# Kernel tuning notes

Hardware: AMD Instinct MI355X
Metric: run time of the kernel (lower is better)

## Reference

```python
import jax, jax.numpy as jnp
import numpy as np

EPS = 1e-5
NUM_HEADS = 4
HEAD_DIM = 64
NUM_STEPS = 3


def layernorm(x, g, b):
    mu = jnp.mean(x, axis=-1, keepdims=True)
    var = jnp.mean((x - mu) ** 2, axis=-1, keepdims=True)
    return (x - mu) / jnp.sqrt(var + EPS) * g + b


def entmax15(x):
    # exact alpha=1.5 entmax along last axis (Peters et al. 2019)
    n = x.shape[-1]
    x = x - jnp.max(x, axis=-1, keepdims=True)
    x = x / 2.0
    srt = -jnp.sort(-x, axis=-1)                      # descending
    rho = jnp.arange(1, n + 1, dtype=x.dtype)
    cs = jnp.cumsum(srt, axis=-1)
    cs2 = jnp.cumsum(srt * srt, axis=-1)
    mean = cs / rho
    ss = cs2 - mean * cs                              # k * (mean_sq - mean^2)
    delta = (1.0 - ss) / rho
    d = jnp.clip(delta, 0.0)
    safe = jnp.where(d > 0, d, 1.0)
    tau = mean - jnp.where(d > 0, jnp.sqrt(safe), 0.0)
    support = (tau <= srt).astype(jnp.int32)
    k_star = jnp.sum(support, axis=-1, keepdims=True) - 1
    tau_star = jnp.take_along_axis(tau, k_star, axis=-1)
    p = jnp.clip(x - tau_star, 0.0)
    return p * p


def setup_inputs() -> dict:
    key = jax.random.key(0)
    ks = jax.random.split(key, 8)
    B, S, Dh = 2, 512, 2048
    N, Dm = 8192, 1024
    T = NUM_HEADS * HEAD_DIM  # 256
    hidden = jax.random.normal(ks[0], (B, S, Dh), dtype=jnp.float32)
    memory = jax.random.normal(ks[1], (N, Dm), dtype=jnp.float32)
    Wq = jax.random.normal(ks[2], (Dh, T), dtype=jnp.float32) * 0.02
    Wk = jax.random.normal(ks[3], (Dm, T), dtype=jnp.float32) * 0.02
    Wv = jax.random.normal(ks[4], (Dm, T), dtype=jnp.float32) * 0.02
    Wo = jax.random.normal(ks[5], (T, Dh), dtype=jnp.float32) * 0.02
    log_beta = jnp.full((NUM_HEADS,), float(np.log(1.0 / np.sqrt(HEAD_DIM))), dtype=jnp.float32)
    g_s = jnp.ones((Dh,), jnp.float32)
    b_s = jnp.zeros((Dh,), jnp.float32)
    g_m = jnp.ones((Dm,), jnp.float32)
    b_m = jnp.zeros((Dm,), jnp.float32)
    return {"hidden": hidden, "memory": memory, "Wq": Wq, "Wk": Wk, "Wv": Wv,
            "Wo": Wo, "log_beta": log_beta, "g_s": g_s, "b_s": b_s,
            "g_m": g_m, "b_m": b_m}


def reference(hidden, memory, Wq, Wk, Wv, Wo, log_beta, g_s, b_s, g_m, b_m):
    B, S, _ = hidden.shape
    N = memory.shape[0]
    H, D = NUM_HEADS, HEAD_DIM
    Q = layernorm(hidden, g_s, b_s) @ Wq                         # [B,S,H*D]
    mem_n = layernorm(memory, g_m, b_m)
    K = (mem_n @ Wk).reshape(N, H, D).transpose(1, 0, 2)         # [H,N,D]
    V = (mem_n @ Wv).reshape(N, H, D).transpose(1, 0, 2)         # [H,N,D]
    xi = Q.reshape(B, S, H, D).transpose(0, 2, 1, 3)             # [B,H,S,D]
    beta = jnp.exp(log_beta)[None, :, None, None]                # [1,H,1,1]
    for _ in range(NUM_STEPS):
        scores = jnp.einsum('bhsd,hnd->bhsn', xi, K) * beta      # [B,H,S,N]
        w = entmax15(scores)
        xi = jnp.einsum('bhsn,hnd->bhsd', w, V)
    converged = xi.transpose(0, 2, 1, 3).reshape(B, S, H * D)
    output = converged @ Wo                                      # [B,S,hidden_dim]
    return output, converged
```

## Files before the change

kernel.cpp:

```cpp
#include <hip/hip_runtime.h>
#include <math.h>

typedef _Float16 f16;
typedef f16 f16x8 __attribute__((ext_vector_type(8)));
typedef float f32x4 __attribute__((ext_vector_type(4)));

#define QSCALE 16384.0f
#define QINV 6.103515625e-5f
#define QOFF 2.5f

__device__ __forceinline__ float wred_add(float v) {
#pragma unroll
  for (int off = 32; off >= 1; off >>= 1) v += __shfl_xor(v, off, 64);
  return v;
}
__device__ __forceinline__ float wred_max(float v) {
#pragma unroll
  for (int off = 32; off >= 1; off >>= 1) v = fmaxf(v, __shfl_xor(v, off, 64));
  return v;
}

__global__ __launch_bounds__(256) void ln_stats_kernel(
    const float* __restrict__ X, int cols, float* __restrict__ mu,
    float* __restrict__ rs) {
  int row = blockIdx.x, tid = threadIdx.x;
  const float4* xr = (const float4*)(X + (size_t)row * cols);
  int nv = cols >> 10;
  float s = 0.f, s2 = 0.f;
  for (int v = 0; v < nv; ++v) {
    float4 x4 = xr[tid + (v << 8)];
    s += x4.x + x4.y + x4.z + x4.w;
    s2 += x4.x * x4.x + x4.y * x4.y + x4.z * x4.z + x4.w * x4.w;
  }
  s = wred_add(s);
  s2 = wred_add(s2);
  __shared__ float rb[8];
  int wid = tid >> 6, lane = tid & 63;
  if (lane == 0) { rb[wid] = s; rb[4 + wid] = s2; }
  __syncthreads();
  if (tid == 0) {
    float S = rb[0] + rb[1] + rb[2] + rb[3];
    float S2 = rb[4] + rb[5] + rb[6] + rb[7];
    float m = S / (float)cols;
    float var = S2 / (float)cols - m * m;
    mu[row] = m;
    rs[row] = 1.f / sqrtf(var + 1e-5f);
  }
}

__global__ __launch_bounds__(256) void split_a_kernel(
    const float* __restrict__ X, const float* __restrict__ mu,
    const float* __restrict__ rs, f16x8* __restrict__ Ah,
    f16x8* __restrict__ Al, int M, int Kd, int lay) {
  int blk = blockIdx.x * 4 + (threadIdx.x >> 6);
  int l = threadIdx.x & 63;
  int nmt = M >> 4;
  int kc = blk / nmt, mt = blk - kc * nmt;
  int m = mt * 16 + (l & 15);
  int k = kc * 32 + ((l >> 4) << 3);
  const float* src;
  if (lay == 0) {
    src = X + (size_t)m * Kd + k;
  } else {
    int b = m >> 9, s = m & 511, hh = k >> 6, d = k & 63;
    src = X + ((((size_t)b * 4 + hh) * 512 + s) << 6) + d;
  }
  float mm = mu ? mu[m] : 0.f;
  float rr = rs ? rs[m] : 1.f;
  f16x8 hi, lo;
#pragma unroll
  for (int j = 0; j < 8; ++j) {
    float v = (src[j] - mm) * rr;
    f16 hv = (f16)v;
    hi[j] = hv;
    lo[j] = (f16)((v - (float)hv) * 512.f);
  }
  size_t o = ((size_t)blk << 6) + l;
  Ah[o] = hi;
  Al[o] = lo;
}

__global__ __launch_bounds__(256) void split_w_kernel(
    const float* __restrict__ W, const float* __restrict__ g,
    f16x8* __restrict__ Bh, f16x8* __restrict__ Bl, int Kd, int N) {
  int blk = blockIdx.x * 4 + (threadIdx.x >> 6);
  int l = threadIdx.x & 63;
  int nnt = N >> 4;
  int kc = blk / nnt, nt = blk - kc * nnt;
  int n = nt * 16 + (l & 15);
  int k0 = kc * 32 + ((l >> 4) << 3);
  f16x8 hi, lo;
#pragma unroll
  for (int j = 0; j < 8; ++j) {
    float v = W[(size_t)(k0 + j) * N + n];
    if (g) v *= g[k0 + j];
    f16 hv = (f16)v;
    hi[j] = hv;
    lo[j] = (f16)((v - (float)hv) * 512.f);
  }
  size_t o = ((size_t)blk << 6) + l;
  Bh[o] = hi;
  Bl[o] = lo;
}

__global__ __launch_bounds__(256) void wcol3_kernel(
    const float* __restrict__ Wq, const float* __restrict__ bq,
    const float* __restrict__ Wk, const float* __restrict__ bk,
    const float* __restrict__ Wv, const float* __restrict__ bv,
    float* __restrict__ vbq, float* __restrict__ vbk,
    float* __restrict__ vbv) {
  int which = blockIdx.z;
  const float* W = which == 0 ? Wq : (which == 1 ? Wk : Wv);
  const float* b = which == 0 ? bq : (which == 1 ? bk : bv);
  float* vb = which == 0 ? vbq : (which == 1 ? vbk : vbv);
  int Kd = which == 0 ? 2048 : 1024;
  int t = threadIdx.x;
  int kpb = Kd >> 4;
  int k0 = blockIdx.y * kpb;
  float s = 0.f;
  for (int k = k0; k < k0 + kpb; ++k) s = fmaf(b[k], W[(size_t)k * 256 + t], s);
  atomicAdd(&vb[t], s);
}

__global__ __launch_bounds__(256) void gemm_mfma_kernel(
    const f16x8* __restrict__ Ah, const f16x8* __restrict__ Al,
    const f16x8* __restrict__ Bh, const f16x8* __restrict__ Bl,
    const float* __restrict__ vb, float* __restrict__ outf,
    f16x8* __restrict__ o16a, f16x8* __restrict__ o16b, int M, int N, int nk,
    int out_mode) {
  __shared__ __align__(16) float Ts[64][68];
  const int tid = threadIdx.x;
  const int w = tid >> 6, l = tid & 63;
  const int ql = l & 15, g = l >> 4;
  const int bn = blockIdx.x, bm = blockIdx.y;
  const size_t astr = ((size_t)(M >> 4)) << 6;
  const size_t bstr = ((size_t)(N >> 4)) << 6;
  const f16x8* aph = Ah + (((size_t)(bm * 4 + w)) << 6) + l;
  const f16x8* apl = Al + (((size_t)(bm * 4 + w)) << 6) + l;
  const f16x8* bph = Bh + (((size_t)(bn * 4)) << 6) + l;
  const f16x8* bpl = Bl + (((size_t)(bn * 4)) << 6) + l;

  f32x4 cm[4], cx[4];
#pragma unroll
  for (int nf = 0; nf < 4; ++nf) {
    cm[nf] = (f32x4){0.f, 0.f, 0.f, 0.f};
    cx[nf] = (f32x4){0.f, 0.f, 0.f, 0.f};
  }

  f16x8 a0h = aph[0], a0l = apl[0];
  f16x8 b0h[4], b0l[4];
#pragma unroll
  for (int nf = 0; nf < 4; ++nf) {
    b0h[nf] = bph[nf << 6];
    b0l[nf] = bpl[nf << 6];
  }

  for (int kc = 0; kc < nk - 1; ++kc) {
    const size_t ao = (size_t)(kc + 1) * astr;
    const size_t bo = (size_t)(kc + 1) * bstr;
    f16x8 a1h = aph[ao], a1l = apl[ao];
    f16x8 b1h[4], b1l[4];
#pragma unroll
    for (int nf = 0; nf < 4; ++nf) {
      b1h[nf] = bph[bo + (nf << 6)];
      b1l[nf] = bpl[bo + (nf << 6)];
    }
#pragma unroll
    for (int nf = 0; nf < 4; ++nf) {
      cm[nf] = __builtin_amdgcn_mfma_f32_16x16x32_f16(a0h, b0h[nf], cm[nf], 0, 0, 0);
      cx[nf] = __builtin_amdgcn_mfma_f32_16x16x32_f16(a0h, b0l[nf], cx[nf], 0, 0, 0);
      cx[nf] = __builtin_amdgcn_mfma_f32_16x16x32_f16(a0l, b0h[nf], cx[nf], 0, 0, 0);
    }
    a0h = a1h;
    a0l = a1l;
#pragma unroll
    for (int nf = 0; nf < 4; ++nf) {
      b0h[nf] = b1h[nf];
      b0l[nf] = b1l[nf];
    }
  }
#pragma unroll
  for (int nf = 0; nf < 4; ++nf) {
    cm[nf] = __builtin_amdgcn_mfma_f32_16x16x32_f16(a0h, b0h[nf], cm[nf], 0, 0, 0);
    cx[nf] = __builtin_amdgcn_mfma_f32_16x16x32_f16(a0h, b0l[nf], cx[nf], 0, 0, 0);
    cx[nf] = __builtin_amdgcn_mfma_f32_16x16x32_f16(a0l, b0h[nf], cx[nf], 0, 0, 0);
  }

  float vbc[4] = {0.f, 0.f, 0.f, 0.f};
  if (vb) {
#pragma unroll
    for (int nf = 0; nf < 4; ++nf) vbc[nf] = vb[bn * 64 + nf * 16 + ql];
  }

  if (out_mode == 0) {
#pragma unroll
    for (int nf = 0; nf < 4; ++nf)
#pragma unroll
      for (int r = 0; r < 4; ++r) {
        float val = fmaf(cx[nf][r], 0.001953125f, cm[nf][r]) + vbc[nf];
        int m = bm * 64 + w * 16 + (g << 2) + r;
        int n = bn * 64 + nf * 16 + ql;
        int b = m >> 9, s = m & 511, hh = n >> 6, d = n & 63;
        outf[((((size_t)b * 4 + hh) * 512 + s) << 6) + d] = val;
      }
  } else if (out_mode == 3) {
#pragma unroll
    for (int nf = 0; nf < 4; ++nf)
#pragma unroll
      for (int r = 0; r < 4; ++r) {
        float val = fmaf(cx[nf][r], 0.001953125f, cm[nf][r]) + vbc[nf];
        int m = bm * 64 + w * 16 + (g << 2) + r;
        int n = bn * 64 + nf * 16 + ql;
        outf[(size_t)m * N + n] = val;
      }
  } else {
#pragma unroll
    for (int nf = 0; nf < 4; ++nf)
#pragma unroll
      for (int r = 0; r < 4; ++r)
        Ts[w * 16 + (g << 2) + r][nf * 16 + ql] =
            fmaf(cx[nf][r], 0.001953125f, cm[nf][r]) + vbc[nf];
    __syncthreads();
    if (out_mode == 4) {
#pragma unroll
      for (int i = 0; i < 2; ++i) {
        int slot = tid + (i << 8);
        int blk = slot >> 6, l2 = slot & 63;
        int ktl = blk >> 1, dc = blk & 1;
        int key = (ktl << 4) + (l2 & 15);
        int db = (dc << 5) + ((l2 >> 4) << 3);
        f16x8 hi, lo;
#pragma unroll
        for (int j = 0; j < 8; ++j) {
          float v = Ts[key][db + j];
          f16 hv = (f16)v;
          hi[j] = hv;
          lo[j] = (f16)((v - (float)hv) * 512.f);
        }
        size_t o = (((size_t)(bn * 512 + bm * 4 + ktl) * 2 + dc) << 6) + l2;
        o16a[o] = hi;
        o16b[o] = lo;
      }
    } else {
#pragma unroll
      for (int i = 0; i < 2; ++i) {
        int slot = tid + (i << 8);
        int blk = slot >> 6, l2 = slot & 63;
        int dt = blk >> 1, kcl = blk & 1;
        int keyb = (kcl << 5) + ((l2 >> 4) << 3);
        int d = (dt << 4) + (l2 & 15);
        f16x8 v8;
#pragma unroll
        for (int j = 0; j < 8; ++j) v8[j] = (f16)Ts[keyb + j][d];
        size_t o = (((size_t)(bn * 4 + dt) * 256 + bm * 2 + kcl) << 6) + l2;
        o16a[o] = v8;
      }
    }
  }
}

__global__ __launch_bounds__(512) void hop_score_kernel(
    const float* __restrict__ xi_in, const f16x8* __restrict__ Khi,
    const f16x8* __restrict__ Klo, const float* __restrict__ log_beta,
    unsigned short* __restrict__ Y) {
  __shared__ float xiq[16][64];
  __shared__ float mxb[8][16];
  __shared__ float mxs[16];
  const int tid = threadIdx.x;
  const int w = tid >> 6, l = tid & 63;
  const int ql = l & 15, g = l >> 4;
  const int bh = blockIdx.x & 7, qtile = blockIdx.x >> 3;
  const int h = bh & 3;
  const size_t base_io = ((size_t)bh * 512 + qtile * 16) * 64;

  float beta = expf(log_beta[h]);
  for (int i = tid; i < 1024; i += 512)
    xiq[i >> 6][i & 63] = xi_in[base_io + i] * beta;
  __syncthreads();

  f16x8 xh0, xh1, xl0, xl1;
#pragma unroll
  for (int j = 0; j < 8; ++j) {
    float x0 = xiq[ql][(g << 3) + j];
    float x1 = xiq[ql][32 + (g << 3) + j];
    f16 h0 = (f16)x0, h1 = (f16)x1;
    xh0[j] = h0; xl0[j] = (f16)((x0 - (float)h0) * 512.f);
    xh1[j] = h1; xl1[j] = (f16)((x1 - (float)h1) * 512.f);
  }

  const f16x8* kb = Khi + (size_t)h * 65536 + l;
  const f16x8* kl = Klo + (size_t)h * 65536 + l;
  const int kt0 = w * 64;

  float mymax = -3.4e38f;
  for (int kt = kt0; kt < kt0 + 2; ++kt) {
    f32x4 c = {0.f, 0.f, 0.f, 0.f};
    c = __builtin_amdgcn_mfma_f32_16x16x32_f16(kb[(size_t)kt * 128], xh0, c, 0, 0, 0);
    c = __builtin_amdgcn_mfma_f32_16x16x32_f16(kb[(size_t)kt * 128 + 64], xh1, c, 0, 0, 0);
    mymax = fmaxf(fmaxf(fmaxf(c[0], c[1]), fmaxf(c[2], c[3])), mymax);
  }
  mymax = fmaxf(mymax, __shfl_xor(mymax, 16, 64));
  mymax = fmaxf(mymax, __shfl_xor(mymax, 32, 64));
  if (l < 16) mxb[w][ql] = mymax;
  __syncthreads();
  if (tid < 16) {
    float m = mxb[0][tid];
#pragma unroll
    for (int ww = 1; ww < 8; ++ww) m = fmaxf(m, mxb[ww][tid]);
    mxs[tid] = m;
  }
  __syncthreads();
  const float mh = mxs[ql] * 0.5f;
  const float qc = QOFF * QSCALE + 0.5f - mh * QSCALE;

  const size_t Ybase = (size_t)(bh * 32 + qtile) * 131072;
  for (int kt = kt0; kt < kt0 + 64; ++kt) {
    f16x8 a0 = kb[(size_t)kt * 128], a1 = kb[(size_t)kt * 128 + 64];
    f16x8 b0 = kl[(size_t)kt * 128], b1 = kl[(size_t)kt * 128 + 64];
    f32x4 cm = {0.f, 0.f, 0.f, 0.f}, cx = {0.f, 0.f, 0.f, 0.f};
    cm = __builtin_amdgcn_mfma_f32_16x16x32_f16(a0, xh0, cm, 0, 0, 0);
    cm = __builtin_amdgcn_mfma_f32_16x16x32_f16(a1, xh1, cm, 0, 0, 0);
    cx = __builtin_amdgcn_mfma_f32_16x16x32_f16(b0, xh0, cx, 0, 0, 0);
    cx = __builtin_amdgcn_mfma_f32_16x16x32_f16(a0, xl0, cx, 0, 0, 0);
    cx = __builtin_amdgcn_mfma_f32_16x16x32_f16(b1, xh1, cx, 0, 0, 0);
    cx = __builtin_amdgcn_mfma_f32_16x16x32_f16(a1, xl1, cx, 0, 0, 0);
    ushort4 uv;
    unsigned short* up = (unsigned short*)&uv;
#pragma unroll
    for (int r = 0; r < 4; ++r) {
      float s = fmaf(cx[r], 0.001953125f, cm[r]);
      float uq = fmaf(s, 8192.0f, qc);
      uq = fminf(fmaxf(uq, 0.f), 65535.f);
      up[r] = (unsigned short)(int)uq;
    }
    *(ushort4*)&Y[Ybase + (size_t)(kt >> 1) * 512 + ql * 32 + (kt & 1) * 16 +
                  (g << 2)] = uv;
  }
}

__global__ __launch_bounds__(256) void hop_tau_kernel(
    const unsigned short* __restrict__ Y, float* __restrict__ tau) {
  const int row = blockIdx.x;
  const int bh = row >> 9, qi = row & 511;
  const int qtile = qi >> 4, ql = qi & 15;
  const size_t yb = (size_t)(bh * 32 + qtile) * 131072 + ql * 32;
  const int t = threadIdx.x;
  const uint4* p = (const uint4*)(Y + yb + (size_t)t * 512);
  float y[32];
#pragma unroll
  for (int v = 0; v < 4; ++v) {
    uint4 u = p[v];
    unsigned a[4] = {u.x, u.y, u.z, u.w};
#pragma unroll
    for (int e = 0; e < 4; ++e) {
      y[v * 8 + e * 2] = fmaf((float)(a[e] & 0xffffu), QINV, -QOFF);
      y[v * 8 + e * 2 + 1] = fmaf((float)(a[e] >> 16), QINV, -QOFF);
    }
  }
  __shared__ float redm[4];
  __shared__ float rb[5][4];
  __shared__ float rb3[3][4][3];
  const int wi = t >> 6, lane = t & 63;

  {
    float m = y[0];
#pragma unroll
    for (int i = 1; i < 32; ++i) m = fmaxf(m, y[i]);
    m = wred_max(m);
    if (lane == 0) redm[wi] = m;
  }
  __syncthreads();
  const float ymax =
      fmaxf(fmaxf(redm[0], redm[1]), fmaxf(redm[2], redm[3]));

  float lo = ymax - 1.001f, hi = ymax;
#pragma unroll 1
  for (int it = 0; it < 5; ++it) {
    float tv = 0.5f * (lo + hi);
    float f = 0.f;
#pragma unroll
    for (int i = 0; i < 32; ++i) {
      float d = fmaxf(y[i] - tv, 0.f);
      f = fmaf(d, d, f);
    }
    f = wred_add(f);
    if (lane == 0) rb[it][wi] = f;
    __syncthreads();
    float tot = rb[it][0] + rb[it][1] + rb[it][2] + rb[it][3];
    if (tot >= 1.f) lo = tv; else hi = tv;
  }

  float tc = lo;
#pragma unroll 1
  for (int it = 0; it < 3; ++it) {
    float kk = 0.f, s1 = 0.f, s2 = 0.f;
#pragma unroll
    for (int i = 0; i < 32; ++i) {
      if (y[i] > tc) { kk += 1.f; s1 += y[i]; s2 = fmaf(y[i], y[i], s2); }
    }
    kk = wred_add(kk);
    s1 = wred_add(s1);
    s2 = wred_add(s2);
    if (lane == 0) { rb3[it][wi][0] = kk; rb3[it][wi][1] = s1; rb3[it][wi][2] = s2; }
    __syncthreads();
    float K = rb3[it][0][0] + rb3[it][1][0] + rb3[it][2][0] + rb3[it][3][0];
    float S1 = rb3[it][0][1] + rb3[it][1][1] + rb3[it][2][1] + rb3[it][3][1];
    float S2 = rb3[it][0][2] + rb3[it][1][2] + rb3[it][2][2] + rb3[it][3][2];
    if (K >= 0.5f) {
      float mean = S1 / K;
      float ss = fmaf(-mean, S1, S2);
      float delta = (1.f - ss) / K;
      tc = delta > 0.f ? mean - sqrtf(delta) : mean;
    }
  }
  if (t == 0) tau[row] = tc;
}

__global__ __launch_bounds__(512) void hop_pv_kernel(
    const unsigned short* __restrict__ Y, const f16x8* __restrict__ Vp,
    const float* __restrict__ tau, float* __restrict__ xi_out) {
  __shared__ float outp[8][16][64];
  __shared__ float taus[16];
  const int tid = threadIdx.x;
  const int w = tid >> 6, l = tid & 63;
  const int ql = l & 15, g = l >> 4;
  const int bh = blockIdx.x & 7, qtile = blockIdx.x >> 3;
  const int h = bh & 3;
  const size_t base_io = ((size_t)bh * 512 + qtile * 16) * 64;

  if (tid < 16) taus[tid] = tau[bh * 512 + qtile * 16 + tid];
  __syncthreads();
  const float t1 = taus[ql];
  const size_t Ybase = (size_t)(bh * 32 + qtile) * 131072;
  const f16x8* vb = Vp + (size_t)h * 65536 + l;

  f32x4 m2[4];
#pragma unroll
  for (int dt = 0; dt < 4; ++dt) m2[dt] = (f32x4){0.f, 0.f, 0.f, 0.f};

  for (int kc = 0; kc < 32; ++kc) {
    const int chunk = w * 32 + kc;
    uint4 uv = *(const uint4*)(Y + Ybase + (size_t)chunk * 512 + ql * 32 +
                               (g << 3));
    unsigned a[4] = {uv.x, uv.y, uv.z, uv.w};
    f16x8 a2;
#pragma unroll
    for (int e = 0; e < 4; ++e) {
      float y0 = fmaf((float)(a[e] & 0xffffu), QINV, -QOFF);
      float y1 = fmaf((float)(a[e] >> 16), QINV, -QOFF);
      float p0 = fmaxf(y0 - t1, 0.f);
      float p1 = fmaxf(y1 - t1, 0.f);
      a2[e * 2] = (f16)(p0 * p0);
      a2[e * 2 + 1] = (f16)(p1 * p1);
    }
#pragma unroll
    for (int dt = 0; dt < 4; ++dt) {
      f16x8 vf = vb[(((size_t)dt * 256 + chunk) << 6)];
      m2[dt] = __builtin_amdgcn_mfma_f32_16x16x32_f16(a2, vf, m2[dt], 0, 0, 0);
    }
  }
#pragma unroll
  for (int dt = 0; dt < 4; ++dt)
#pragma unroll
    for (int r = 0; r < 4; ++r)
      outp[w][(g << 2) + r][dt * 16 + ql] = m2[dt][r];
  __syncthreads();
  for (int i = tid; i < 1024; i += 512) {
    float s = 0.f;
#pragma unroll
    for (int ww = 0; ww < 8; ++ww) s += outp[ww][i >> 6][i & 63];
    xi_out[base_io + i] = s;
  }
}

__global__ __launch_bounds__(256) void conv_copy_kernel(
    const float* __restrict__ xi, float* __restrict__ out) {
  int o4 = blockIdx.x * 256 + threadIdx.x;
  int o = o4 << 2;
  int dd = o & 63, hq = (o >> 6) & 3, sq = (o >> 8) & 511, bq = o >> 17;
  float4 v =
      *(const float4*)&xi[((((size_t)bq << 2) + hq) * 512 + sq) * 64 + dd];
  *(float4*)&out[o] = v;
}

extern "C" void kernel_launch(void* const* d_in, const int* in_sizes, int n_in,
                              void* d_out, int out_size, void* d_ws,
                              size_t ws_size, hipStream_t stream) {
  (void)in_sizes; (void)n_in; (void)out_size; (void)ws_size;
  const float* hidden = (const float*)d_in[0];
  const float* memory = (const float*)d_in[1];
  const float* Wq = (const float*)d_in[2];
  const float* Wk = (const float*)d_in[3];
  const float* Wv = (const float*)d_in[4];
  const float* Wo = (const float*)d_in[5];
  const float* log_beta = (const float*)d_in[6];
  const float* g_s = (const float*)d_in[7];
  const float* b_s = (const float*)d_in[8];
  const float* g_m = (const float*)d_in[9];
  const float* b_m = (const float*)d_in[10];
  float* out = (float*)d_out;

  float* ws = (float*)d_ws;
  float* mu_h = ws;
  float* rs_h = ws + 1024;
  float* mu_m = ws + 2048;
  float* rs_m = ws + 10240;
  float* xiA = ws + 18432;
  float* xiB = ws + 280576;
  float* vb_q = ws + 542720;
  float* vb_k = ws + 542976;
  float* vb_v = ws + 543232;
  float* tau = ws + 543488;
  f16x8* Khi = (f16x8*)(ws + 548864);
  f16x8* Klo = Khi + 262144;
  f16x8* Vp = Klo + 262144;
  f16x8* Bqh = Vp + 262144;
  f16x8* Bql = Bqh + 65536;
  f16x8* Bkh = Bql + 65536;
  f16x8* Bkl = Bkh + 32768;
  f16x8* Bvh = Bkl + 32768;
  f16x8* Bvl = Bvh + 32768;
  f16x8* Boh = Bvl + 32768;
  f16x8* Bol = Boh + 65536;
  unsigned short* Y = (unsigned short*)(Bol + 65536);
  f16x8* Amh = (f16x8*)Y;
  f16x8* Aml = Amh + 1048576;
  f16x8* Ahh = Aml + 1048576;
  f16x8* Ahl = Ahh + 262144;
  f16x8* Axh = Ahl + 262144;
  f16x8* Axl = Axh + 32768;

  ln_stats_kernel<<<1024, 256, 0, stream>>>(hidden, 2048, mu_h, rs_h);
  ln_stats_kernel<<<8192, 256, 0, stream>>>(memory, 1024, mu_m, rs_m);
  hipMemsetAsync(vb_q, 0, 3 * 256 * sizeof(float), stream);

  split_a_kernel<<<1024, 256, 0, stream>>>(hidden, mu_h, rs_h, Ahh, Ahl, 1024,
                                           2048, 0);
  split_a_kernel<<<4096, 256, 0, stream>>>(memory, mu_m, rs_m, Amh, Aml, 8192,
                                           1024, 0);
  split_w_kernel<<<256, 256, 0, stream>>>(Wq, g_s, Bqh, Bql, 2048, 256);
  split_w_kernel<<<128, 256, 0, stream>>>(Wk, g_m, Bkh, Bkl, 1024, 256);
  split_w_kernel<<<128, 256, 0, stream>>>(Wv, g_m, Bvh, Bvl, 1024, 256);
  split_w_kernel<<<256, 256, 0, stream>>>(Wo, nullptr, Boh, Bol, 256, 2048);
  wcol3_kernel<<<dim3(1, 16, 3), 256, 0, stream>>>(Wq, b_s, Wk, b_m, Wv, b_m,
                                                   vb_q, vb_k, vb_v);

  gemm_mfma_kernel<<<dim3(4, 16), 256, 0, stream>>>(
      Ahh, Ahl, Bqh, Bql, vb_q, xiA, nullptr, nullptr, 1024, 256, 64, 0);
  gemm_mfma_kernel<<<dim3(4, 128), 256, 0, stream>>>(
      Amh, Aml, Bkh, Bkl, vb_k, nullptr, Khi, Klo, 8192, 256, 32, 4);
  gemm_mfma_kernel<<<dim3(4, 128), 256, 0, stream>>>(
      Amh, Aml, Bvh, Bvl, vb_v, nullptr, Vp, nullptr, 8192, 256, 32, 5);

  float* xin = xiA;
  float* xout = xiB;
  for (int step = 0; step < 3; ++step) {
    hop_score_kernel<<<256, 512, 0, stream>>>(xin, Khi, Klo, log_beta, Y);
    hop_tau_kernel<<<4096, 256, 0, stream>>>(Y, tau);
    hop_pv_kernel<<<256, 512, 0, stream>>>(Y, Vp, tau, xout);
    float* t = xin; xin = xout; xout = t;
  }

  split_a_kernel<<<128, 256, 0, stream>>>(xin, nullptr, nullptr, Axh, Axl,
                                          1024, 256, 1);
  gemm_mfma_kernel<<<dim3(32, 16), 256, 0, stream>>>(
      Axh, Axl, Boh, Bol, nullptr, out, nullptr, nullptr, 1024, 2048, 8, 3);
  conv_copy_kernel<<<256, 256, 0, stream>>>(xin, out + 2097152);
}
```

Before: 462.6 us.

## Merge setup launches and widen entmax tau kernel to 512 threads

Merges the two layernorm-stat launches into one and the four weight-split launches into one, which cuts per-launch overhead. The tau kernel now runs 512 threads per row, each holding 16 scalar values in registers instead of a 32-entry array. Its refinement loop accumulates the shifted sums d=max(y-tc,0) and rebuilds S1 and S2 algebraically. The aims are more parallelism and lower register pressure, at the cost of reducing across 8 waves instead of 4 and some floating-point risk in the shifted-sum reconstruction.

After: 499.3 us. +7.9%, slower.

```diff
diff --git a/kernel.cpp b/kernel.cpp
--- a/kernel.cpp
+++ b/kernel.cpp
@@ -20,10 +20,17 @@
   return v;
 }
 
-__global__ __launch_bounds__(256) void ln_stats_kernel(
-    const float* __restrict__ X, int cols, float* __restrict__ mu,
-    float* __restrict__ rs) {
-  int row = blockIdx.x, tid = threadIdx.x;
+__global__ __launch_bounds__(256) void ln_stats_all_kernel(
+    const float* __restrict__ hidden, const float* __restrict__ memory,
+    float* __restrict__ mu_h, float* __restrict__ rs_h,
+    float* __restrict__ mu_m, float* __restrict__ rs_m) {
+  int b = blockIdx.x, tid = threadIdx.x;
+  const float* X;
+  float* mu;
+  float* rs;
+  int cols, row;
+  if (b < 1024) { X = hidden; cols = 2048; mu = mu_h; rs = rs_h; row = b; }
+  else { X = memory; cols = 1024; mu = mu_m; rs = rs_m; row = b - 1024; }
   const float4* xr = (const float4*)(X + (size_t)row * cols);
   int nv = cols >> 10;
   float s = 0.f, s2 = 0.f;
@@ -80,10 +87,24 @@
   Al[o] = lo;
 }
 
-__global__ __launch_bounds__(256) void split_w_kernel(
-    const float* __restrict__ W, const float* __restrict__ g,
-    f16x8* __restrict__ Bh, f16x8* __restrict__ Bl, int Kd, int N) {
-  int blk = blockIdx.x * 4 + (threadIdx.x >> 6);
+__global__ __launch_bounds__(256) void split_w_all_kernel(
+    const float* __restrict__ Wq, const float* __restrict__ Wk,
+    const float* __restrict__ Wv, const float* __restrict__ Wo,
+    const float* __restrict__ g_s, const float* __restrict__ g_m,
+    f16x8* __restrict__ Bqh, f16x8* __restrict__ Bql,
+    f16x8* __restrict__ Bkh, f16x8* __restrict__ Bkl,
+    f16x8* __restrict__ Bvh, f16x8* __restrict__ Bvl,
+    f16x8* __restrict__ Boh, f16x8* __restrict__ Bol) {
+  int b = blockIdx.x;
+  const float* W;
+  const float* g;
+  f16x8 *Bh, *Bl;
+  int N, base;
+  if (b < 256) { W = Wq; g = g_s; Bh = Bqh; Bl = Bql; N = 256; base = 0; }
+  else if (b < 384) { W = Wk; g = g_m; Bh = Bkh; Bl = Bkl; N = 256; base = 256; }
+  else if (b < 512) { W = Wv; g = g_m; Bh = Bvh; Bl = Bvl; N = 256; base = 384; }
+  else { W = Wo; g = nullptr; Bh = Boh; Bl = Bol; N = 2048; base = 512; }
+  int blk = (b - base) * 4 + (threadIdx.x >> 6);
   int l = threadIdx.x & 63;
   int nnt = N >> 4;
   int kc = blk / nnt, nt = blk - kc * nnt;
@@ -338,75 +359,92 @@
   }
 }
 
-__global__ __launch_bounds__(256) void hop_tau_kernel(
+#define TAU_EACH(OP)                                                        \
+  OP(y0) OP(y1) OP(y2) OP(y3) OP(y4) OP(y5) OP(y6) OP(y7)                   \
+  OP(y8) OP(y9) OP(y10) OP(y11) OP(y12) OP(y13) OP(y14) OP(y15)
+#define OPMX(v) m = fmaxf(m, (v));
+#define OPBI(v) { float d = fmaxf((v) - tv, 0.f); f = fmaf(d, d, f); }
+#define OPRF(v)                                                             \
+  { float d = fmaxf((v) - tc, 0.f);                                         \
+    sd += d; sd2 = fmaf(d, d, sd2); cnt += (d > 0.f) ? 1.f : 0.f; }
+
+__global__ __launch_bounds__(512, 2) void hop_tau_kernel(
     const unsigned short* __restrict__ Y, float* __restrict__ tau) {
   const int row = blockIdx.x;
   const int bh = row >> 9, qi = row & 511;
   const int qtile = qi >> 4, ql = qi & 15;
   const size_t yb = (size_t)(bh * 32 + qtile) * 131072 + ql * 32;
   const int t = threadIdx.x;
-  const uint4* p = (const uint4*)(Y + yb + (size_t)t * 512);
-  float y[32];
-#pragma unroll
-  for (int v = 0; v < 4; ++v) {
-    uint4 u = p[v];
-    unsigned a[4] = {u.x, u.y, u.z, u.w};
-#pragma unroll
-    for (int e = 0; e < 4; ++e) {
-      y[v * 8 + e * 2] = fmaf((float)(a[e] & 0xffffu), QINV, -QOFF);
-      y[v * 8 + e * 2 + 1] = fmaf((float)(a[e] >> 16), QINV, -QOFF);
-    }
-  }
-  __shared__ float redm[4];
-  __shared__ float rb[5][4];
-  __shared__ float rb3[3][4][3];
   const int wi = t >> 6, lane = t & 63;
 
-  {
-    float m = y[0];
-#pragma unroll
-    for (int i = 1; i < 32; ++i) m = fmaxf(m, y[i]);
-    m = wred_max(m);
-    if (lane == 0) redm[wi] = m;
-  }
+  const uint4* p =
+      (const uint4*)(Y + yb + (size_t)(t >> 1) * 512 + (t & 1) * 16);
+  uint4 u0 = p[0], u1 = p[1];
+  float y0 = fmaf((float)(u0.x & 0xffffu), QINV, -QOFF);
+  float y1 = fmaf((float)(u0.x >> 16), QINV, -QOFF);
+  float y2 = fmaf((float)(u0.y & 0xffffu), QINV, -QOFF);
+  float y3 = fmaf((float)(u0.y >> 16), QINV, -QOFF);
+  float y4 = fmaf((float)(u0.z & 0xffffu), QINV, -QOFF);
+  float y5 = fmaf((float)(u0.z >> 16), QINV, -QOFF);
+  float y6 = fmaf((float)(u0.w & 0xffffu), QINV, -QOFF);
+  float y7 = fmaf((float)(u0.w >> 16), QINV, -QOFF);
+  float y8 = fmaf((float)(u1.x & 0xffffu), QINV, -QOFF);
+  float y9 = fmaf((float)(u1.x >> 16), QINV, -QOFF);
+  float y10 = fmaf((float)(u1.y & 0xffffu), QINV, -QOFF);
+  float y11 = fmaf((float)(u1.y >> 16), QINV, -QOFF);
+  float y12 = fmaf((float)(u1.z & 0xffffu), QINV, -QOFF);
+  float y13 = fmaf((float)(u1.z >> 16), QINV, -QOFF);
+  float y14 = fmaf((float)(u1.w & 0xffffu), QINV, -QOFF);
+  float y15 = fmaf((float)(u1.w >> 16), QINV, -QOFF);
+
+  __shared__ float redm[8];
+  __shared__ float rb[5][8];
+  __shared__ float rb3[3][8][3];
+
+  float m = y0;
+  TAU_EACH(OPMX)
+  m = wred_max(m);
+  if (lane == 0) redm[wi] = m;
   __syncthreads();
-  const float ymax =
-      fmaxf(fmaxf(redm[0], redm[1]), fmaxf(redm[2], redm[3]));
+  float ymax = redm[0];
+#pragma unroll
+  for (int s = 1; s < 8; ++s) ymax = fmaxf(ymax, redm[s]);
 
   float lo = ymax - 1.001f, hi = ymax;
 #pragma unroll 1
   for (int it = 0; it < 5; ++it) {
     float tv = 0.5f * (lo + hi);
     float f = 0.f;
-#pragma unroll
-    for (int i = 0; i < 32; ++i) {
-      float d = fmaxf(y[i] - tv, 0.f);
-      f = fmaf(d, d, f);
-    }
+    TAU_EACH(OPBI)
     f = wred_add(f);
     if (lane == 0) rb[it][wi] = f;
     __syncthreads();
-    float tot = rb[it][0] + rb[it][1] + rb[it][2] + rb[it][3];
+    float tot = 0.f;
+#pragma unroll
+    for (int s = 0; s < 8; ++s) tot += rb[it][s];
     if (tot >= 1.f) lo = tv; else hi = tv;
   }
 
   float tc = lo;
 #pragma unroll 1
   for (int it = 0; it < 3; ++it) {
-    float kk = 0.f, s1 = 0.f, s2 = 0.f;
-#pragma unroll
-    for (int i = 0; i < 32; ++i) {
-      if (y[i] > tc) { kk += 1.f; s1 += y[i]; s2 = fmaf(y[i], y[i], s2); }
-    }
-    kk = wred_add(kk);
-    s1 = wred_add(s1);
-    s2 = wred_add(s2);
-    if (lane == 0) { rb3[it][wi][0] = kk; rb3[it][wi][1] = s1; rb3[it][wi][2] = s2; }
+    float cnt = 0.f, sd = 0.f, sd2 = 0.f;
+    TAU_EACH(OPRF)
+    cnt = wred_add(cnt);
+    sd = wred_add(sd);
+    sd2 = wred_add(sd2);
+    if (lane == 0) {
+      rb3[it][wi][0] = cnt; rb3[it][wi][1] = sd; rb3[it][wi][2] = sd2;
+    }
     __syncthreads();
-    float K = rb3[it][0][0] + rb3[it][1][0] + rb3[it][2][0] + rb3[it][3][0];
-    float S1 = rb3[it][0][1] + rb3[it][1][1] + rb3[it][2][1] + rb3[it][3][1];
-    float S2 = rb3[it][0][2] + rb3[it][1][2] + rb3[it][2][2] + rb3[it][3][2];
+    float K = 0.f, SD = 0.f, SD2 = 0.f;
+#pragma unroll
+    for (int s = 0; s < 8; ++s) {
+      K += rb3[it][s][0]; SD += rb3[it][s][1]; SD2 += rb3[it][s][2];
+    }
     if (K >= 0.5f) {
+      float S1 = SD + K * tc;
+      float S2 = SD2 + 2.f * tc * S1 - tc * tc * K;
       float mean = S1 / K;
       float ss = fmaf(-mean, S1, S2);
       float delta = (1.f - ss) / K;
@@ -530,18 +568,17 @@
   f16x8* Axh = Ahl + 262144;
   f16x8* Axl = Axh + 32768;
 
-  ln_stats_kernel<<<1024, 256, 0, stream>>>(hidden, 2048, mu_h, rs_h);
-  ln_stats_kernel<<<8192, 256, 0, stream>>>(memory, 1024, mu_m, rs_m);
+  ln_stats_all_kernel<<<9216, 256, 0, stream>>>(hidden, memory, mu_h, rs_h,
+                                                mu_m, rs_m);
   hipMemsetAsync(vb_q, 0, 3 * 256 * sizeof(float), stream);
 
   split_a_kernel<<<1024, 256, 0, stream>>>(hidden, mu_h, rs_h, Ahh, Ahl, 1024,
                                            2048, 0);
   split_a_kernel<<<4096, 256, 0, stream>>>(memory, mu_m, rs_m, Amh, Aml, 8192,
                                            1024, 0);
-  split_w_kernel<<<256, 256, 0, stream>>>(Wq, g_s, Bqh, Bql, 2048, 256);
-  split_w_kernel<<<128, 256, 0, stream>>>(Wk, g_m, Bkh, Bkl, 1024, 256);
-  split_w_kernel<<<128, 256, 0, stream>>>(Wv, g_m, Bvh, Bvl, 1024, 256);
-  split_w_kernel<<<256, 256, 0, stream>>>(Wo, nullptr, Boh, Bol, 256, 2048);
+  split_w_all_kernel<<<768, 256, 0, stream>>>(Wq, Wk, Wv, Wo, g_s, g_m, Bqh,
+                                              Bql, Bkh, Bkl, Bvh, Bvl, Boh,
+                                              Bol);
   wcol3_kernel<<<dim3(1, 16, 3), 256, 0, stream>>>(Wq, b_s, Wk, b_m, Wv, b_m,
                                                    vb_q, vb_k, vb_v);
 
@@ -556,7 +593,7 @@
   float* xout = xiB;
   for (int step = 0; step < 3; ++step) {
     hop_score_kernel<<<256, 512, 0, stream>>>(xin, Khi, Klo, log_beta, Y);
-    hop_tau_kernel<<<4096, 256, 0, stream>>>(Y, tau);
+    hop_tau_kernel<<<4096, 512, 0, stream>>>(Y, tau);
     hop_pv_kernel<<<256, 512, 0, stream>>>(Y, Vp, tau, xout);
     float* t = xin; xin = xout; xout = t;
   }
```
